# Kernel tuning notes

Hardware: AMD Instinct MI355X
Metric: run time of the kernel (lower is better)

The kernel has to match this reference:

```python
import jax, jax.numpy as jnp
import numpy as np
from jax.ops import segment_sum

N_NODES = 50000
N_EDGES = 800000


def _gcn_layer(h, src, dst, W, b, norm_out, norm_in, activation):
    # DGL GraphConv, norm='both': scale by src out-deg^-1/2, transform, aggregate, scale by dst in-deg^-1/2
    h = h * norm_out[:, None]
    h = h @ W                              # transform first (out dim smaller) -> cheaper messages
    msg = h[src]                           # [E, d_out] irregular gather
    agg = segment_sum(msg, dst, num_segments=h.shape[0])  # [N, d_out] scatter-add
    out = agg * norm_in[:, None] + b
    if activation is not None:
        out = activation(out)
    return out


def setup_inputs() -> dict:
    key = jax.random.key(0)
    ks = jax.random.split(key, 6)
    feat = jax.random.normal(ks[0], (N_NODES, 256), dtype=jnp.float32)
    src = jax.random.randint(ks[1], (N_EDGES,), 0, N_NODES, dtype=jnp.int32)
    dst = jax.random.randint(ks[2], (N_EDGES,), 0, N_NODES, dtype=jnp.int32)
    W1 = jax.random.normal(ks[3], (256, 64), dtype=jnp.float32) * (1.0 / np.sqrt(256))
    b1 = jnp.zeros((64,), dtype=jnp.float32)
    W2 = jax.random.normal(ks[4], (64, 40), dtype=jnp.float32) * (1.0 / np.sqrt(64))
    b2 = jnp.zeros((40,), dtype=jnp.float32)
    return {"feat": feat, "src": src, "dst": dst, "W1": W1, "b1": b1, "W2": W2, "b2": b2}


def reference(feat, src, dst, W1, b1, W2, b2):
    n = feat.shape[0]
    ones = jnp.ones((src.shape[0],), dtype=feat.dtype)
    deg_out = segment_sum(ones, src, num_segments=n)
    deg_in = segment_sum(ones, dst, num_segments=n)
    # DGL clamps degrees to min 1 (allow_zero_in_degree=True)
    norm_out = jnp.maximum(deg_out, 1.0) ** -0.5
    norm_in = jnp.maximum(deg_in, 1.0) ** -0.5
    h = _gcn_layer(feat, src, dst, W1, b1, norm_out, norm_in, jax.nn.relu)
    # dropout is identity in inference
    h = _gcn_layer(h, src, dst, W2, b2, norm_out, norm_in, None)
    return h
```

## Files before the change

kernel.cpp:

```cpp
#include <hip/hip_runtime.h>
#include <stdint.h>

#define N_NODES 50000
#define N_EDGES 800000
#define D_IN    256
#define D_H     64
#define D_O     40

#define NB_H   256
#define NT_H   512
#define EPB    (N_EDGES / NB_H)
#define BINS_W 12500

typedef unsigned int u32;
typedef unsigned short u16;
typedef unsigned char u8;
typedef __bf16 bf16;
typedef __attribute__((ext_vector_type(8))) __bf16 bf16x8;
typedef __attribute__((ext_vector_type(4))) float f32x4;


__global__ void __launch_bounds__(NT_H) hist_both_kernel(const int* __restrict__ src,
                                                         const int* __restrict__ dst,
                                                         u32* __restrict__ part_s,
                                                         u32* __restrict__ part_d) {
    __shared__ u32 bins[BINS_W];
    const int gb = blockIdx.x;
    const int b = (gb < NB_H) ? gb : gb - NB_H;
    const int* __restrict__ idx = (gb < NB_H) ? src : dst;
    u32* __restrict__ part = (gb < NB_H) ? part_s : part_d;
    const int e0 = b * EPB;
    const int e1 = (e0 + EPB < N_EDGES) ? e0 + EPB : N_EDGES;
    for (int i = threadIdx.x; i < BINS_W; i += NT_H) bins[i] = 0;
    __syncthreads();
    for (int e = e0 + threadIdx.x; e < e1; e += NT_H) {
        int v = idx[e];
        atomicAdd(&bins[v >> 2], 1u << ((v & 3) * 8));
    }
    __syncthreads();
    for (int i = threadIdx.x; i < BINS_W; i += NT_H)
        part[(size_t)b * BINS_W + i] = bins[i];
}


#define SCAN_NB ((N_NODES + 255) / 256)

__global__ void norm_both_kernel(const u8* __restrict__ part_s8,
                                 u8* __restrict__ part_d8,
                                 float* __restrict__ norm_out,
                                 float* __restrict__ norm_in,
                                 int* __restrict__ start,
                                 int* __restrict__ blocksum) {
    __shared__ int tmp[256];
    const int half = blockIdx.x < SCAN_NB ? 0 : 1;
    if (half == 0) {
        const int n = blockIdx.x * 256 + threadIdx.x;
        if (n >= N_NODES) return;
        u32 acc = 0;
#pragma unroll 8
        for (int b = 0; b < NB_H; ++b) acc += part_s8[(size_t)b * N_NODES + n];
        norm_out[n] = rsqrtf(fmaxf((float)acc, 1.0f));
    } else {
        const int blk = blockIdx.x - SCAN_NB;
        const int n = blk * 256 + threadIdx.x;
        u32 acc = 0;
        if (n < N_NODES) {
#pragma unroll 8
            for (int b = 0; b < NB_H; ++b) {
                size_t i = (size_t)b * N_NODES + n;
                u8 t = part_d8[i];
                part_d8[i] = (u8)acc;
                acc += t;
            }
            norm_in[n] = rsqrtf(fmaxf((float)acc, 1.0f));
        }
        int v = (int)acc;
        tmp[threadIdx.x] = v;
        __syncthreads();
        for (int off = 1; off < 256; off <<= 1) {
            int t = (threadIdx.x >= off) ? tmp[threadIdx.x - off] : 0;
            __syncthreads();
            tmp[threadIdx.x] += t;
            __syncthreads();
        }
        if (n < N_NODES) start[n] = tmp[threadIdx.x] - v;
        if (threadIdx.x == 255) blocksum[blk] = tmp[255];
    }
}


__global__ void scan2_kernel(int* __restrict__ blocksum) {
    __shared__ int tmp[256];
    int v = (threadIdx.x < SCAN_NB) ? blocksum[threadIdx.x] : 0;
    tmp[threadIdx.x] = v;
    __syncthreads();
    for (int off = 1; off < 256; off <<= 1) {
        int t = (threadIdx.x >= off) ? tmp[threadIdx.x - off] : 0;
        __syncthreads();
        tmp[threadIdx.x] += t;
        __syncthreads();
    }
    blocksum[threadIdx.x] = tmp[threadIdx.x] - v;
}

__global__ void scan3_kernel(int* __restrict__ start, const int* __restrict__ blocksum) {
    int i = blockIdx.x * 256 + threadIdx.x;
    if (i < N_NODES) start[i] += blocksum[i >> 8];
    if (i == 0) start[N_NODES] = N_EDGES;
}


__global__ void __launch_bounds__(NT_H) scatter2_kernel(const int* __restrict__ src,
                                                        const int* __restrict__ dst,
                                                        const int* __restrict__ start,
                                                        const u8* __restrict__ off8,
                                                        u16* __restrict__ ssrc) {
    __shared__ u32 cur[BINS_W];
    const int b = blockIdx.x;
    const int e0 = b * EPB;
    const int e1 = (e0 + EPB < N_EDGES) ? e0 + EPB : N_EDGES;
    for (int i = threadIdx.x; i < BINS_W; i += NT_H) cur[i] = 0;
    __syncthreads();
    for (int e = e0 + threadIdx.x; e < e1; e += NT_H) {
        int d = dst[e];
        int sh = (d & 3) * 8;
        u32 old = atomicAdd(&cur[d >> 2], 1u << sh);
        int c = (int)((old >> sh) & 0xFFu);
        int pos = start[d] + (int)off8[(size_t)b * N_NODES + d] + c;
        ssrc[pos] = (u16)src[e];
    }
}


#define AST 40

__global__ void __launch_bounds__(256, 4) gemm1_kernel(const float* __restrict__ feat,
                                                       const float* __restrict__ W1,
                                                       const float* __restrict__ norm_out,
                                                       bf16* __restrict__ h1) {
    __shared__ __align__(16) bf16 Ah[2][64 * AST];
    __shared__ __align__(16) bf16 Al[2][64 * AST];
    __shared__ __align__(16) bf16 Wh[2][64 * AST];

    const int tid = threadIdx.x;
    const int lane = tid & 63;
    const int wv = __builtin_amdgcn_readfirstlane(tid >> 6);
    const int n0 = blockIdx.x * 64;

    const int ar = tid >> 2;
    const int ak = (tid & 3) * 8;
    int nra = n0 + ar; if (nra >= N_NODES) nra = N_NODES - 1;
    const float* asrc = feat + (size_t)nra * D_IN + ak;

    const int wcol = tid & 63;
    const int wk0 = (tid >> 6) * 8;
    const float* wsrc = W1 + wcol;

    f32x4 acc[4];
#pragma unroll
    for (int ct = 0; ct < 4; ++ct) acc[ct] = (f32x4){0.f, 0.f, 0.f, 0.f};

    const int fr = lane & 15;
    const int fg = (lane >> 4) * 8;

    auto stageA = [&](int buf, int s) {
        float4 a0 = *(const float4*)(asrc + s * 32);
        float4 a1 = *(const float4*)(asrc + s * 32 + 4);
        float av[8] = {a0.x, a0.y, a0.z, a0.w, a1.x, a1.y, a1.z, a1.w};
        bf16x8 H, L;
#pragma unroll
        for (int j = 0; j < 8; ++j) {
            bf16 h = (bf16)av[j];
            H[j] = h;
            L[j] = (bf16)(av[j] - (float)h);
        }
        *(bf16x8*)&Ah[buf][ar * AST + ak] = H;
        *(bf16x8*)&Al[buf][ar * AST + ak] = L;
    };

    auto stageW = [&](int buf, int s) {
        float wv8[8];
#pragma unroll
        for (int j = 0; j < 8; ++j)
            wv8[j] = wsrc[(size_t)(s * 32 + wk0 + j) * D_H];
        bf16x8 H;
#pragma unroll
        for (int j = 0; j < 8; ++j) H[j] = (bf16)wv8[j];
        *(bf16x8*)&Wh[buf][wcol * AST + wk0] = H;
    };

    auto compute = [&](int buf) {
        bf16x8 ah = *(const bf16x8*)&Ah[buf][(wv * 16 + fr) * AST + fg];
        bf16x8 al = *(const bf16x8*)&Al[buf][(wv * 16 + fr) * AST + fg];
#pragma unroll
        for (int ct = 0; ct < 4; ++ct) {
            bf16x8 bh = *(const bf16x8*)&Wh[buf][(ct * 16 + fr) * AST + fg];
            acc[ct] = __builtin_amdgcn_mfma_f32_16x16x32_bf16(ah, bh, acc[ct], 0, 0, 0);
            acc[ct] = __builtin_amdgcn_mfma_f32_16x16x32_bf16(al, bh, acc[ct], 0, 0, 0);
        }
    };

    stageA(0, 0);
    stageW(0, 0);
    __syncthreads();
#pragma unroll
    for (int s = 0; s < 8; ++s) {
        const int buf = s & 1;
        if (s < 7) {
            stageA(buf ^ 1, s + 1);
            stageW(buf ^ 1, s + 1);
        }
        compute(buf);
        __syncthreads();
    }

    const int orow = n0 + wv * 16 + (lane >> 4) * 4;
    const int ocol = lane & 15;
    float nrm[4];
#pragma unroll
    for (int r = 0; r < 4; ++r)
        nrm[r] = (orow + r < N_NODES) ? norm_out[orow + r] : 0.0f;
#pragma unroll
    for (int ct = 0; ct < 4; ++ct) {
#pragma unroll
        for (int r = 0; r < 4; ++r) {
            if (orow + r < N_NODES)
                h1[(size_t)(orow + r) * D_H + ct * 16 + ocol] = (bf16)(acc[ct][r] * nrm[r]);
        }
    }
}


__global__ void __launch_bounds__(256) agg1_kernel(const int* __restrict__ start,
                                                   const u16* __restrict__ ssrc,
                                                   const bf16* __restrict__ h1,
                                                   const float* __restrict__ norm_in,
                                                   const float* __restrict__ norm_out,
                                                   const float* __restrict__ b1,
                                                   bf16* __restrict__ g) {
    const int lane = threadIdx.x & 63;
    const int c = lane & 7;
    const int t = lane >> 3;
    const int n = (int)((blockIdx.x * blockDim.x + threadIdx.x) >> 6);
    if (n >= N_NODES) return;

    int beg = __builtin_amdgcn_readfirstlane(start[n]);
    int end = __builtin_amdgcn_readfirstlane(start[n + 1]);
    float acc[8];
#pragma unroll
    for (int j = 0; j < 8; ++j) acc[j] = 0.0f;

    for (int e = beg + t; e < end; e += 16) {
        int s0 = ssrc[e];
        bf16x8 v0 = *(const bf16x8*)(h1 + (size_t)s0 * D_H + c * 8);
        if (e + 8 < end) {
            int s1 = ssrc[e + 8];
            bf16x8 v1 = *(const bf16x8*)(h1 + (size_t)s1 * D_H + c * 8);
#pragma unroll
            for (int j = 0; j < 8; ++j) acc[j] += (float)v1[j];
        }
#pragma unroll
        for (int j = 0; j < 8; ++j) acc[j] += (float)v0[j];
    }
#pragma unroll
    for (int j = 0; j < 8; ++j) {
        acc[j] += __shfl_xor(acc[j], 8);
        acc[j] += __shfl_xor(acc[j], 16);
        acc[j] += __shfl_xor(acc[j], 32);
    }
    if (t == 0) {
        float ni = norm_in[n], no = norm_out[n];
        float4 b0 = *(const float4*)&b1[c * 8];
        float4 b1v = *(const float4*)&b1[c * 8 + 4];
        bf16x8 r;
        r[0] = (bf16)(fmaxf(fmaf(acc[0], ni, b0.x), 0.f) * no);
        r[1] = (bf16)(fmaxf(fmaf(acc[1], ni, b0.y), 0.f) * no);
        r[2] = (bf16)(fmaxf(fmaf(acc[2], ni, b0.z), 0.f) * no);
        r[3] = (bf16)(fmaxf(fmaf(acc[3], ni, b0.w), 0.f) * no);
        r[4] = (bf16)(fmaxf(fmaf(acc[4], ni, b1v.x), 0.f) * no);
        r[5] = (bf16)(fmaxf(fmaf(acc[5], ni, b1v.y), 0.f) * no);
        r[6] = (bf16)(fmaxf(fmaf(acc[6], ni, b1v.z), 0.f) * no);
        r[7] = (bf16)(fmaxf(fmaf(acc[7], ni, b1v.w), 0.f) * no);
        *(bf16x8*)(g + (size_t)n * D_H + c * 8) = r;
    }
}


#define AST2 72

__global__ void __launch_bounds__(256, 4) gemm2_kernel(const bf16* __restrict__ g,
                                                       const float* __restrict__ W2,
                                                       bf16* __restrict__ h2) {
    __shared__ __align__(16) bf16 Ah[64 * AST2];
    __shared__ __align__(16) bf16 Wh[48 * AST2];
    __shared__ __align__(16) bf16 Wl[48 * AST2];

    const int tid = threadIdx.x;
    const int lane = tid & 63;
    const int wv = __builtin_amdgcn_readfirstlane(tid >> 6);
    const int n0 = blockIdx.x * 64;

    {
        const int ar = tid >> 2;
        const int ak = (tid & 3) * 16;
        int nra = n0 + ar; if (nra >= N_NODES) nra = N_NODES - 1;
        const bf16* asrc = g + (size_t)nra * D_H + ak;
        *(bf16x8*)&Ah[ar * AST2 + ak]     = *(const bf16x8*)(asrc);
        *(bf16x8*)&Ah[ar * AST2 + ak + 8] = *(const bf16x8*)(asrc + 8);
    }
    if (tid < 192) {
        const int col = tid >> 2;
        const int k0 = (tid & 3) * 16;
        float wv16[16];
#pragma unroll
        for (int j = 0; j < 16; ++j)
            wv16[j] = (col < D_O) ? W2[(size_t)(k0 + j) * D_O + col] : 0.0f;
        bf16x8 H0, L0, H1, L1;
#pragma unroll
        for (int j = 0; j < 8; ++j) {
            bf16 h = (bf16)wv16[j];
            H0[j] = h; L0[j] = (bf16)(wv16[j] - (float)h);
            bf16 hb = (bf16)wv16[j + 8];
            H1[j] = hb; L1[j] = (bf16)(wv16[j + 8] - (float)hb);
        }
        *(bf16x8*)&Wh[col * AST2 + k0] = H0;
        *(bf16x8*)&Wh[col * AST2 + k0 + 8] = H1;
        *(bf16x8*)&Wl[col * AST2 + k0] = L0;
        *(bf16x8*)&Wl[col * AST2 + k0 + 8] = L1;
    }
    __syncthreads();

    const int fr = lane & 15;
    const int fg = (lane >> 4) * 8;

    f32x4 acc[3];
#pragma unroll
    for (int ct = 0; ct < 3; ++ct) acc[ct] = (f32x4){0.f, 0.f, 0.f, 0.f};

#pragma unroll
    for (int s = 0; s < 2; ++s) {
        bf16x8 ah = *(const bf16x8*)&Ah[(wv * 16 + fr) * AST2 + s * 32 + fg];
#pragma unroll
        for (int ct = 0; ct < 3; ++ct) {
            bf16x8 bh = *(const bf16x8*)&Wh[(ct * 16 + fr) * AST2 + s * 32 + fg];
            bf16x8 bl = *(const bf16x8*)&Wl[(ct * 16 + fr) * AST2 + s * 32 + fg];
            acc[ct] = __builtin_amdgcn_mfma_f32_16x16x32_bf16(ah, bh, acc[ct], 0, 0, 0);
            acc[ct] = __builtin_amdgcn_mfma_f32_16x16x32_bf16(ah, bl, acc[ct], 0, 0, 0);
        }
    }

    const int orow = n0 + wv * 16 + (lane >> 4) * 4;
    const int ocol = lane & 15;
#pragma unroll
    for (int ct = 0; ct < 3; ++ct) {
        int col = ct * 16 + ocol;
        if (col < D_O) {
#pragma unroll
            for (int r = 0; r < 4; ++r) {
                if (orow + r < N_NODES)
                    h2[(size_t)(orow + r) * D_O + col] = (bf16)acc[ct][r];
            }
        }
    }
}


__global__ void __launch_bounds__(256) agg2_kernel(const int* __restrict__ start,
                                                   const u16* __restrict__ ssrc,
                                                   const bf16* __restrict__ h2,
                                                   const float* __restrict__ norm_in,
                                                   const float* __restrict__ b2,
                                                   float* __restrict__ out) {
    const int lane = threadIdx.x & 63;
    const int c = lane & 7;
    const int t = lane >> 3;
    const int n = (int)((blockIdx.x * blockDim.x + threadIdx.x) >> 6);
    if (n >= N_NODES) return;

    int beg = __builtin_amdgcn_readfirstlane(start[n]);
    int end = __builtin_amdgcn_readfirstlane(start[n + 1]);
    float acc[8];
#pragma unroll
    for (int j = 0; j < 8; ++j) acc[j] = 0.0f;

    if (c < 5) {
        for (int e = beg + t; e < end; e += 16) {
            int s0 = ssrc[e];
            bf16x8 v0 = *(const bf16x8*)(h2 + (size_t)s0 * D_O + c * 8);
            if (e + 8 < end) {
                int s1 = ssrc[e + 8];
                bf16x8 v1 = *(const bf16x8*)(h2 + (size_t)s1 * D_O + c * 8);
#pragma unroll
                for (int j = 0; j < 8; ++j) acc[j] += (float)v1[j];
            }
#pragma unroll
            for (int j = 0; j < 8; ++j) acc[j] += (float)v0[j];
        }
    }
#pragma unroll
    for (int j = 0; j < 8; ++j) {
        acc[j] += __shfl_xor(acc[j], 8);
        acc[j] += __shfl_xor(acc[j], 16);
        acc[j] += __shfl_xor(acc[j], 32);
    }
    if (t == 0 && c < 5) {
        float ni = norm_in[n];
        float4 b0 = *(const float4*)&b2[c * 8];
        float4 b1v = *(const float4*)&b2[c * 8 + 4];
        float* op = out + (size_t)n * D_O + c * 8;
        *(float4*)(op) = make_float4(fmaf(acc[0], ni, b0.x), fmaf(acc[1], ni, b0.y),
                                     fmaf(acc[2], ni, b0.z), fmaf(acc[3], ni, b0.w));
        *(float4*)(op + 4) = make_float4(fmaf(acc[4], ni, b1v.x), fmaf(acc[5], ni, b1v.y),
                                         fmaf(acc[6], ni, b1v.z), fmaf(acc[7], ni, b1v.w));
    }
}


static inline char* alignup(char* p, size_t a) {
    return (char*)(((uintptr_t)p + a - 1) & ~(uintptr_t)(a - 1));
}

extern "C" void kernel_launch(void* const* d_in, const int* in_sizes, int n_in,
                              void* d_out, int out_size, void* d_ws, size_t ws_size,
                              hipStream_t stream) {
    const float* feat = (const float*)d_in[0];
    const int*   src  = (const int*)d_in[1];
    const int*   dst  = (const int*)d_in[2];
    const float* W1   = (const float*)d_in[3];
    const float* b1   = (const float*)d_in[4];
    const float* W2   = (const float*)d_in[5];
    const float* b2   = (const float*)d_in[6];
    float* out = (float*)d_out;

    char* p = alignup((char*)d_ws, 256);
    int*   start    = (int*)p;    p = alignup(p + (N_NODES + 1) * 4, 256);
    int*   blocksum = (int*)p;    p = alignup(p + 256 * 4, 256);
    float* norm_out = (float*)p;  p = alignup(p + N_NODES * 4, 256);
    float* norm_in  = (float*)p;  p = alignup(p + N_NODES * 4, 256);
    u16*   ssrc     = (u16*)p;    p = alignup(p + N_EDGES * 2, 256);
    bf16*  h1       = (bf16*)p;   p = alignup(p + (size_t)N_NODES * D_H * 2, 256);
    bf16*  g        = (bf16*)p;   p = alignup(p + (size_t)N_NODES * D_H * 2, 256);
    bf16*  h2q     = (bf16*)p;    p = alignup(p + (size_t)N_NODES * D_O * 2, 256);
    u32*   part_s   = (u32*)p;    p = alignup(p + (size_t)NB_H * BINS_W * 4, 256);
    u32*   part_d   = (u32*)p;    p = alignup(p + (size_t)NB_H * BINS_W * 4, 256);

    hist_both_kernel<<<2 * NB_H, NT_H, 0, stream>>>(src, dst, part_s, part_d);
    norm_both_kernel<<<2 * SCAN_NB, 256, 0, stream>>>((const u8*)part_s, (u8*)part_d,
                                                      norm_out, norm_in, start, blocksum);
    scan2_kernel<<<1, 256, 0, stream>>>(blocksum);
    scan3_kernel<<<SCAN_NB, 256, 0, stream>>>(start, blocksum);

    scatter2_kernel<<<NB_H, NT_H, 0, stream>>>(src, dst, start, (const u8*)part_d, ssrc);

    gemm1_kernel<<<(N_NODES + 63) / 64, 256, 0, stream>>>(feat, W1, norm_out, h1);
    agg1_kernel<<<(N_NODES + 3) / 4, 256, 0, stream>>>(start, ssrc, h1, norm_in, norm_out, b1, g);

    gemm2_kernel<<<(N_NODES + 63) / 64, 256, 0, stream>>>(g, W2, h2q);
    agg2_kernel<<<(N_NODES + 3) / 4, 256, 0, stream>>>(start, ssrc, h2q, norm_in, b2, out);
}
```

Measured before the change: 113.6 us.

## Pack degree reductions by u32 words, merge scan kernels, pre-convert W1 to bf16

```diff
diff --git a/kernel.cpp b/kernel.cpp
--- a/kernel.cpp
+++ b/kernel.cpp
@@ -11,6 +11,7 @@
 #define NT_H   512
 #define EPB    (N_EDGES / NB_H)
 #define BINS_W 12500
+#define NBLK1  ((BINS_W + 255) / 256)
 
 typedef unsigned int u32;
 typedef unsigned short u16;
@@ -23,9 +24,23 @@
 __global__ void __launch_bounds__(NT_H) hist_both_kernel(const int* __restrict__ src,
                                                          const int* __restrict__ dst,
                                                          u32* __restrict__ part_s,
-                                                         u32* __restrict__ part_d) {
+                                                         u32* __restrict__ part_d,
+                                                         const float* __restrict__ W1,
+                                                         bf16* __restrict__ W1t) {
     __shared__ u32 bins[BINS_W];
     const int gb = blockIdx.x;
+    if (gb >= 2 * NB_H) {
+        int t = (gb - 2 * NB_H) * NT_H + threadIdx.x;
+        int c = t & 63;
+        int kq = t >> 6;
+        int k0 = kq * 8;
+        bf16x8 H;
+#pragma unroll
+        for (int j = 0; j < 8; ++j)
+            H[j] = (bf16)W1[(size_t)(k0 + j) * D_H + c];
+        *(bf16x8*)&W1t[(size_t)kq * 512 + c * 8] = H;
+        return;
+    }
     const int b = (gb < NB_H) ? gb : gb - NB_H;
     const int* __restrict__ idx = (gb < NB_H) ? src : dst;
     u32* __restrict__ part = (gb < NB_H) ? part_s : part_d;
@@ -43,70 +58,95 @@
 }
 
 
-#define SCAN_NB ((N_NODES + 255) / 256)
-
-__global__ void norm_both_kernel(const u8* __restrict__ part_s8,
-                                 u8* __restrict__ part_d8,
+__global__ void norm_both_kernel(const u32* __restrict__ part_s,
+                                 u32* __restrict__ part_d,
                                  float* __restrict__ norm_out,
                                  float* __restrict__ norm_in,
                                  int* __restrict__ start,
                                  int* __restrict__ blocksum) {
     __shared__ int tmp[256];
-    const int half = blockIdx.x < SCAN_NB ? 0 : 1;
-    if (half == 0) {
-        const int n = blockIdx.x * 256 + threadIdx.x;
-        if (n >= N_NODES) return;
-        u32 acc = 0;
+    const int tid = threadIdx.x;
+    if (blockIdx.x < NBLK1) {
+        const int n4 = blockIdx.x * 256 + tid;
+        if (n4 >= BINS_W) return;
+        u32 a02 = 0, a13 = 0;
 #pragma unroll 8
-        for (int b = 0; b < NB_H; ++b) acc += part_s8[(size_t)b * N_NODES + n];
-        norm_out[n] = rsqrtf(fmaxf((float)acc, 1.0f));
+        for (int b = 0; b < NB_H; ++b) {
+            u32 w = part_s[(size_t)b * BINS_W + n4];
+            a02 += w & 0x00FF00FFu;
+            a13 += (w >> 8) & 0x00FF00FFu;
+        }
+        float4 no;
+        no.x = rsqrtf(fmaxf((float)(a02 & 0xFFFFu), 1.0f));
+        no.y = rsqrtf(fmaxf((float)(a13 & 0xFFFFu), 1.0f));
+        no.z = rsqrtf(fmaxf((float)(a02 >> 16), 1.0f));
+        no.w = rsqrtf(fmaxf((float)(a13 >> 16), 1.0f));
+        *(float4*)&norm_out[(size_t)n4 * 4] = no;
     } else {
-        const int blk = blockIdx.x - SCAN_NB;
-        const int n = blk * 256 + threadIdx.x;
-        u32 acc = 0;
-        if (n < N_NODES) {
+        const int blk = blockIdx.x - NBLK1;
+        const int n4 = blk * 256 + tid;
+        const bool ok = (n4 < BINS_W);
+        u32 a02 = 0, a13 = 0;
+        if (ok) {
 #pragma unroll 8
             for (int b = 0; b < NB_H; ++b) {
-                size_t i = (size_t)b * N_NODES + n;
-                u8 t = part_d8[i];
-                part_d8[i] = (u8)acc;
-                acc += t;
+                size_t i = (size_t)b * BINS_W + n4;
+                u32 w = part_d[i];
+                u32 off = (a02 & 0xFFu) | ((a13 & 0xFFu) << 8) |
+                          (a02 & 0xFF0000u) | ((a13 & 0xFF0000u) << 8);
+                part_d[i] = off;
+                a02 += w & 0x00FF00FFu;
+                a13 += (w >> 8) & 0x00FF00FFu;
             }
-            norm_in[n] = rsqrtf(fmaxf((float)acc, 1.0f));
-        }
-        int v = (int)acc;
-        tmp[threadIdx.x] = v;
+        }
+        const int d0 = (int)(a02 & 0xFFFFu), d1 = (int)(a13 & 0xFFFFu);
+        const int d2 = (int)(a02 >> 16),    d3 = (int)(a13 >> 16);
+        if (ok) {
+            float4 ni;
+            ni.x = rsqrtf(fmaxf((float)d0, 1.0f));
+            ni.y = rsqrtf(fmaxf((float)d1, 1.0f));
+            ni.z = rsqrtf(fmaxf((float)d2, 1.0f));
+            ni.w = rsqrtf(fmaxf((float)d3, 1.0f));
+            *(float4*)&norm_in[(size_t)n4 * 4] = ni;
+        }
+        int s = ok ? (d0 + d1 + d2 + d3) : 0;
+        tmp[tid] = s;
         __syncthreads();
         for (int off = 1; off < 256; off <<= 1) {
-            int t = (threadIdx.x >= off) ? tmp[threadIdx.x - off] : 0;
+            int t = (tid >= off) ? tmp[tid - off] : 0;
             __syncthreads();
-            tmp[threadIdx.x] += t;
+            tmp[tid] += t;
             __syncthreads();
         }
-        if (n < N_NODES) start[n] = tmp[threadIdx.x] - v;
-        if (threadIdx.x == 255) blocksum[blk] = tmp[255];
-    }
-}
-
-
-__global__ void scan2_kernel(int* __restrict__ blocksum) {
-    __shared__ int tmp[256];
-    int v = (threadIdx.x < SCAN_NB) ? blocksum[threadIdx.x] : 0;
-    tmp[threadIdx.x] = v;
-    __syncthreads();
-    for (int off = 1; off < 256; off <<= 1) {
-        int t = (threadIdx.x >= off) ? tmp[threadIdx.x - off] : 0;
-        __syncthreads();
-        tmp[threadIdx.x] += t;
-        __syncthreads();
-    }
-    blocksum[threadIdx.x] = tmp[threadIdx.x] - v;
-}
-
-__global__ void scan3_kernel(int* __restrict__ start, const int* __restrict__ blocksum) {
-    int i = blockIdx.x * 256 + threadIdx.x;
-    if (i < N_NODES) start[i] += blocksum[i >> 8];
-    if (i == 0) start[N_NODES] = N_EDGES;
+        if (ok) {
+            int P = tmp[tid] - s;
+            int4 st;
+            st.x = P;
+            st.y = P + d0;
+            st.z = P + d0 + d1;
+            st.w = P + d0 + d1 + d2;
+            *(int4*)&start[(size_t)n4 * 4] = st;
+        }
+        if (tid == 255) blocksum[blk] = tmp[255];
+    }
+}
+
+
+__global__ void scan23_kernel(int* __restrict__ start, const int* __restrict__ blocksum) {
+    __shared__ int pre[NBLK1];
+    if (threadIdx.x == 0) {
+        int a = 0;
+        for (int b = 0; b < NBLK1; ++b) { pre[b] = a; a += blocksum[b]; }
+    }
+    __syncthreads();
+    const int add = pre[blockIdx.x];
+    const int n4 = blockIdx.x * 256 + threadIdx.x;
+    if (n4 < BINS_W) {
+        int4 v = *(int4*)&start[(size_t)n4 * 4];
+        v.x += add; v.y += add; v.z += add; v.w += add;
+        *(int4*)&start[(size_t)n4 * 4] = v;
+    }
+    if (blockIdx.x == 0 && threadIdx.x == 0) start[N_NODES] = N_EDGES;
 }
 
 
@@ -135,7 +175,7 @@
 #define AST 40
 
 __global__ void __launch_bounds__(256, 4) gemm1_kernel(const float* __restrict__ feat,
-                                                       const float* __restrict__ W1,
+                                                       const bf16* __restrict__ W1t,
                                                        const float* __restrict__ norm_out,
                                                        bf16* __restrict__ h1) {
     __shared__ __align__(16) bf16 Ah[2][64 * AST];
@@ -154,7 +194,7 @@
 
     const int wcol = tid & 63;
     const int wk0 = (tid >> 6) * 8;
-    const float* wsrc = W1 + wcol;
+    const int wkq = tid >> 6;
 
     f32x4 acc[4];
 #pragma unroll
@@ -179,14 +219,8 @@
     };
 
     auto stageW = [&](int buf, int s) {
-        float wv8[8];
-#pragma unroll
-        for (int j = 0; j < 8; ++j)
-            wv8[j] = wsrc[(size_t)(s * 32 + wk0 + j) * D_H];
-        bf16x8 H;
-#pragma unroll
-        for (int j = 0; j < 8; ++j) H[j] = (bf16)wv8[j];
-        *(bf16x8*)&Wh[buf][wcol * AST + wk0] = H;
+        *(bf16x8*)&Wh[buf][wcol * AST + wk0] =
+            *(const bf16x8*)(W1t + ((size_t)(s * 4 + wkq) * 512 + wcol * 8));
     };
 
     auto compute = [&](int buf) {
@@ -437,22 +471,22 @@
     int*   blocksum = (int*)p;    p = alignup(p + 256 * 4, 256);
     float* norm_out = (float*)p;  p = alignup(p + N_NODES * 4, 256);
     float* norm_in  = (float*)p;  p = alignup(p + N_NODES * 4, 256);
+    bf16*  W1t      = (bf16*)p;   p = alignup(p + (size_t)D_IN * D_H * 2, 256);
     u16*   ssrc     = (u16*)p;    p = alignup(p + N_EDGES * 2, 256);
     bf16*  h1       = (bf16*)p;   p = alignup(p + (size_t)N_NODES * D_H * 2, 256);
     bf16*  g        = (bf16*)p;   p = alignup(p + (size_t)N_NODES * D_H * 2, 256);
-    bf16*  h2q     = (bf16*)p;    p = alignup(p + (size_t)N_NODES * D_O * 2, 256);
+    bf16*  h2q      = (bf16*)p;   p = alignup(p + (size_t)N_NODES * D_O * 2, 256);
     u32*   part_s   = (u32*)p;    p = alignup(p + (size_t)NB_H * BINS_W * 4, 256);
     u32*   part_d   = (u32*)p;    p = alignup(p + (size_t)NB_H * BINS_W * 4, 256);
 
-    hist_both_kernel<<<2 * NB_H, NT_H, 0, stream>>>(src, dst, part_s, part_d);
-    norm_both_kernel<<<2 * SCAN_NB, 256, 0, stream>>>((const u8*)part_s, (u8*)part_d,
-                                                      norm_out, norm_in, start, blocksum);
-    scan2_kernel<<<1, 256, 0, stream>>>(blocksum);
-    scan3_kernel<<<SCAN_NB, 256, 0, stream>>>(start, blocksum);
+    hist_both_kernel<<<2 * NB_H + 4, NT_H, 0, stream>>>(src, dst, part_s, part_d, W1, W1t);
+    norm_both_kernel<<<2 * NBLK1, 256, 0, stream>>>(part_s, part_d, norm_out, norm_in,
+                                                    start, blocksum);
+    scan23_kernel<<<NBLK1, 256, 0, stream>>>(start, blocksum);
 
     scatter2_kernel<<<NB_H, NT_H, 0, stream>>>(src, dst, start, (const u8*)part_d, ssrc);
 
-    gemm1_kernel<<<(N_NODES + 63) / 64, 256, 0, stream>>>(feat, W1, norm_out, h1);
+    gemm1_kernel<<<(N_NODES + 63) / 64, 256, 0, stream>>>(feat, W1t, norm_out, h1);
     agg1_kernel<<<(N_NODES + 3) / 4, 256, 0, stream>>>(start, ssrc, h1, norm_in, norm_out, b1, g);
 
     gemm2_kernel<<<(N_NODES + 63) / 64, 256, 0, stream>>>(g, W2, h2q);
```

Measured after the change: 113.5 us. No clear change (-0.1%).
